# Kernel tuning notes

Hardware: AMD Instinct MI355X
Metric: run time of the kernel (lower is better)

Reference implementation:

```python
import jax, jax.numpy as jnp
import numpy as np

D_MODEL = 1024
NUM_HEADS = 16
HEAD_DIM = D_MODEL // NUM_HEADS
SCALE = HEAD_DIM ** -0.5


def setup_inputs() -> dict:
    key = jax.random.key(0)
    ks = jax.random.split(key, 5)
    B, N = 2, 2048
    x = jax.random.normal(ks[0], (B, N, D_MODEL), dtype=jnp.float32)
    # Linear params, torch layout: weight [out, in], bias [out]
    w_qkv = jax.random.normal(ks[1], (3 * D_MODEL, D_MODEL), dtype=jnp.float32) * (D_MODEL ** -0.5)
    b_qkv = jax.random.normal(ks[2], (3 * D_MODEL,), dtype=jnp.float32) * 0.02
    w_proj = jax.random.normal(ks[3], (D_MODEL, D_MODEL), dtype=jnp.float32) * (D_MODEL ** -0.5)
    b_proj = jax.random.normal(ks[4], (D_MODEL,), dtype=jnp.float32) * 0.02
    return {"x": x, "w_qkv": w_qkv, "b_qkv": b_qkv, "w_proj": w_proj, "b_proj": b_proj}


def reference(x, w_qkv, b_qkv, w_proj, b_proj):
    B, N, C = x.shape
    qkv = x @ w_qkv.T + b_qkv                      # [B, N, 3C]
    qkv = qkv.reshape(B, N, 3, NUM_HEADS, HEAD_DIM)
    qkv = jnp.transpose(qkv, (2, 0, 3, 1, 4))      # [3, B, H, N, d]
    q, k, v = qkv[0], qkv[1], qkv[2]
    attn = jnp.einsum('bhnd,bhmd->bhnm', q, k) * SCALE  # [B, H, N, N]
    attn = jax.nn.softmax(attn, axis=-1)
    # dropout is identity in eval mode
    out = jnp.einsum('bhnm,bhmd->bhnd', attn, v)   # [B, H, N, d]
    out = jnp.transpose(out, (0, 2, 1, 3)).reshape(B, N, C)
    return out @ w_proj.T + b_proj
```

## Files before the change

### kernel.cpp

```cpp
#include <hip/hip_runtime.h>

typedef short short8 __attribute__((ext_vector_type(8)));
typedef short short4v __attribute__((ext_vector_type(4)));
typedef float f32x4 __attribute__((ext_vector_type(4)));
typedef float float4v __attribute__((ext_vector_type(4)));
typedef int int4v __attribute__((ext_vector_type(4)));
typedef int int2v __attribute__((ext_vector_type(2)));

__device__ __forceinline__ short f2bf(float f) {
  union { float f; unsigned u; } v; v.f = f;
  unsigned r = v.u + 0x7FFFu + ((v.u >> 16) & 1u);
  return (short)(r >> 16);
}

__device__ __forceinline__ unsigned cvtpk_bf16(float lo, float hi) {
  unsigned r;
  asm("v_cvt_pk_bf16_f32 %0, %1, %2" : "=v"(r) : "v"(lo), "v"(hi));
  return r;
}

#define GLD16(gp, lp)                                                   \
  __builtin_amdgcn_global_load_lds(                                     \
      (const __attribute__((address_space(1))) void*)(gp),              \
      (__attribute__((address_space(3))) void*)(lp), 16, 0, 0)

#define QSCALE 0.18033688011112042f

__global__ __launch_bounds__(256) void cvt_all(
    const float* __restrict__ x, const float* __restrict__ wq, const float* __restrict__ wp,
    short* __restrict__ xb, short* __restrict__ wqb, short* __restrict__ wpb) {
  int i = blockIdx.x * 256 + threadIdx.x;
  const float* s; short* d; int off;
  if (i < 1048576)      { s = x;  d = xb;  off = i; }
  else if (i < 1835008) { s = wq; d = wqb; off = i - 1048576; }
  else                  { s = wp; d = wpb; off = i - 1835008; }
  float4v v = ((const float4v*)s)[off];
  short4v o;
  o.x = f2bf(v.x); o.y = f2bf(v.y); o.z = f2bf(v.z); o.w = f2bf(v.w);
  ((short4v*)d)[off] = o;
}

template <int MODE>
__global__ __launch_bounds__(256) void gemm_bt(
    const short* __restrict__ A, const short* __restrict__ Bw,
    const float* __restrict__ bias,
    short* __restrict__ qo, short* __restrict__ ko, short* __restrict__ vto,
    float* __restrict__ outf) {
  __shared__ short As[2][128 * 64];
  __shared__ short Bs[2][128 * 64];
  const int t = threadIdx.x;
  const int lane = t & 63, wid = t >> 6;
  const int g = lane >> 4, l15 = lane & 15;
  const int wr = (wid >> 1) * 64, wc = (wid & 1) * 64;
  const int bm0 = blockIdx.y * 128, bn0 = blockIdx.x * 128;

  const int sr = t >> 3;
  const int ssub0 = t & 7;

  const int swz = (l15 & 7) << 4;
  int aoff[2][4], boff[2][4];
#pragma unroll
  for (int kk = 0; kk < 2; ++kk)
#pragma unroll
    for (int f = 0; f < 4; ++f) {
      aoff[kk][f] = ((wr + f * 16 + l15) * 128 + kk * 64 + g * 16) ^ swz;
      boff[kk][f] = ((wc + f * 16 + l15) * 128 + kk * 64 + g * 16) ^ swz;
    }

  f32x4 acc[4][4] = {};

  auto stage = [&](int buf, int k0) {
#pragma unroll
    for (int i = 0; i < 4; ++i) {
      int row = i * 32 + sr;
      int s = ssub0 ^ (row & 7);
      char* ldsA = (char*)&As[buf][0] + (i * 256 + (t & ~63)) * 16;
      char* ldsB = (char*)&Bs[buf][0] + (i * 256 + (t & ~63)) * 16;
      GLD16(A + (size_t)(bm0 + row) * 1024 + k0 + s * 8, ldsA);
      GLD16(Bw + (size_t)(bn0 + row) * 1024 + k0 + s * 8, ldsB);
    }
  };

  stage(0, 0);
  stage(1, 64);
  int curOff = 0;

  for (int it = 0; it < 16; ++it) {
    if (it == 15) asm volatile("s_waitcnt vmcnt(0)" ::: "memory");
    else          asm volatile("s_waitcnt vmcnt(8)" ::: "memory");
    __builtin_amdgcn_s_barrier();
    __builtin_amdgcn_sched_barrier(0);
    const char* AsB = (const char*)&As[0][0] + curOff;
    const char* BsB = (const char*)&Bs[0][0] + curOff;
#pragma unroll
    for (int kk = 0; kk < 2; ++kk) {
      short8 a[4], b[4];
#pragma unroll
      for (int mi = 0; mi < 4; ++mi) a[mi] = *(const short8*)(AsB + aoff[kk][mi]);
#pragma unroll
      for (int ni = 0; ni < 4; ++ni) b[ni] = *(const short8*)(BsB + boff[kk][ni]);
#pragma unroll
      for (int mi = 0; mi < 4; ++mi)
#pragma unroll
        for (int ni = 0; ni < 4; ++ni)
          acc[mi][ni] = __builtin_amdgcn_mfma_f32_16x16x32_bf16(a[mi], b[ni], acc[mi][ni], 0, 0, 0);
    }
    __builtin_amdgcn_sched_barrier(0);
    __builtin_amdgcn_s_barrier();
    __builtin_amdgcn_sched_barrier(0);
    if (it + 2 < 16) stage(it & 1, (it + 2) * 64);
    curOff ^= 16384;
  }

  if constexpr (MODE == 0) {
    const int which = bn0 >> 10;
    if (which == 2) {
#pragma unroll
      for (int mi = 0; mi < 4; ++mi) {
#pragma unroll
        for (int ni = 0; ni < 4; ++ni) {
          int gcol = bn0 + wc + ni * 16 + l15;
          int w1 = gcol & 1023;
          int h = w1 >> 6, dd = w1 & 63;
          float bv = bias[gcol];
          int grow0 = bm0 + wr + mi * 16 + g * 4;
          int b_ = grow0 >> 11, n0 = grow0 & 2047;
          int bh = b_ * 16 + h;
          int nl = n0 & 63;
          int np = (n0 & ~63) | (nl & 32) | ((nl & 12) << 1) | ((nl & 16) >> 2);
          int2v pk;
          pk.x = (int)cvtpk_bf16(acc[mi][ni][0] + bv, acc[mi][ni][1] + bv);
          pk.y = (int)cvtpk_bf16(acc[mi][ni][2] + bv, acc[mi][ni][3] + bv);
          *(int2v*)(vto + ((size_t)bh * 64 + dd) * 2048 + np) = pk;
        }
      }
    } else {
      short* dst = (which == 0) ? qo : ko;
      const float sc = (which == 0) ? QSCALE : 1.0f;
#pragma unroll
      for (int mi = 0; mi < 4; ++mi) {
#pragma unroll
        for (int ni = 0; ni < 4; ++ni) {
          int gcol = bn0 + wc + ni * 16 + l15;
          int w1 = gcol & 1023;
          int h = w1 >> 6, dd = w1 & 63;
          float bv = bias[gcol];
#pragma unroll
          for (int r = 0; r < 4; ++r) {
            int grow = bm0 + wr + mi * 16 + g * 4 + r;
            int b_ = grow >> 11, n = grow & 2047;
            int bh = b_ * 16 + h;
            dst[((size_t)bh * 2048 + n) * 64 + dd] = f2bf((acc[mi][ni][r] + bv) * sc);
          }
        }
      }
    }
  } else {
#pragma unroll
    for (int mi = 0; mi < 4; ++mi) {
#pragma unroll
      for (int ni = 0; ni < 4; ++ni) {
        int gcol = bn0 + wc + ni * 16 + l15;
        float bv = bias[gcol];
#pragma unroll
        for (int r = 0; r < 4; ++r) {
          int grow = bm0 + wr + mi * 16 + g * 4 + r;
          outf[(size_t)grow * 1024 + gcol] = acc[mi][ni][r] + bv;
        }
      }
    }
  }
}

__global__ __launch_bounds__(256, 2) void attn_fused(
    const short* __restrict__ Qg, const short* __restrict__ Kg,
    const short* __restrict__ Vtg, short* __restrict__ AO) {
  __shared__ short Ks[4][64 * 64];
  __shared__ short Vs[4][64 * 64];
  const int bid = blockIdx.x;
  const int bh = bid & 31, qt = bid >> 5;
  const int t = threadIdx.x, wid = t >> 6, lane = t & 63;
  const int g = lane >> 4, l15 = lane & 15;
  const int q0w = qt * 128 + wid * 32;
  const short* qb = Qg + ((size_t)bh * 2048 + q0w) * 64;
  const short* kb = Kg + (size_t)bh * 2048 * 64;
  const short* vb = Vtg + (size_t)bh * 64 * 2048;

  const int srow = t >> 3;
  const int ssub = (t & 7) ^ (srow & 7);
  const short* ksrc0 = kb + srow * 64 + ssub * 8;
  const short* vsrc0 = vb + (size_t)srow * 2048 + ssub * 8;

  const int swz = (l15 & 7) << 4;
  int foff[2][4];
#pragma unroll
  for (int kk = 0; kk < 2; ++kk)
#pragma unroll
    for (int f = 0; f < 4; ++f)
      foff[kk][f] = ((f * 16 + l15) * 128 + kk * 64 + g * 16) ^ swz;

  short8 bq[2][2];
#pragma unroll
  for (int qf = 0; qf < 2; ++qf)
#pragma unroll
    for (int kk = 0; kk < 2; ++kk)
      bq[qf][kk] = *(const short8*)(qb + (qf * 16 + l15) * 64 + kk * 32 + g * 8);

  auto stageP = [&](int buf, int p) {
    const int n0 = p * 128;
#pragma unroll
    for (int sub = 0; sub < 2; ++sub) {
      const int nn = n0 + sub * 64;
      char* ldsK = (char*)&Ks[buf * 2 + sub][0] + wid * 1024;
      char* ldsV = (char*)&Vs[buf * 2 + sub][0] + wid * 1024;
#pragma unroll
      for (int i = 0; i < 2; ++i) {
        GLD16(ksrc0 + (size_t)(nn + i * 32) * 64, ldsK + i * 4096);
        GLD16(vsrc0 + (size_t)i * 32 * 2048 + nn, ldsV + i * 4096);
      }
    }
  };

  stageP(0, 0);
  stageP(1, 1);

  f32x4 acc[2][4] = {};
  float mrun[2] = {-3.0e38f, -3.0e38f}, lrun[2] = {0.f, 0.f};

  for (int p = 0; p < 16; ++p) {
    if (p == 15) asm volatile("s_waitcnt vmcnt(0)" ::: "memory");
    else         asm volatile("s_waitcnt vmcnt(8)" ::: "memory");
    __builtin_amdgcn_s_barrier();
    __builtin_amdgcn_sched_barrier(0);
    const int buf = p & 1;

#pragma unroll
    for (int sub = 0; sub < 2; ++sub) {
      const char* KsB = (const char*)&Ks[buf * 2 + sub][0];
      const char* VsB = (const char*)&Vs[buf * 2 + sub][0];

      f32x4 s[2][4] = {};
#pragma unroll
      for (int kk = 0; kk < 2; ++kk) {
        short8 ak[4];
#pragma unroll
        for (int kf = 0; kf < 4; ++kf) ak[kf] = *(const short8*)(KsB + foff[kk][kf]);
#pragma unroll
        for (int kf = 0; kf < 4; ++kf)
#pragma unroll
          for (int qf = 0; qf < 2; ++qf)
            s[qf][kf] = __builtin_amdgcn_mfma_f32_16x16x32_bf16(ak[kf], bq[qf][kk], s[qf][kf], 0, 0, 0);
      }

      float pm[2];
#pragma unroll
      for (int qf = 0; qf < 2; ++qf) {
        float m0 = fmaxf(s[qf][0][0], s[qf][0][1]);
        m0 = fmaxf(fmaxf(m0, s[qf][0][2]), s[qf][0][3]);
#pragma unroll
        for (int kf = 1; kf < 4; ++kf) {
          m0 = fmaxf(fmaxf(m0, s[qf][kf][0]), s[qf][kf][1]);
          m0 = fmaxf(fmaxf(m0, s[qf][kf][2]), s[qf][kf][3]);
        }
        float x = fmaxf(m0, __shfl_xor(m0, 16));
        pm[qf] = fmaxf(x, __shfl_xor(x, 32));
      }

      if (!__all((pm[0] - mrun[0] <= 8.f) && (pm[1] - mrun[1] <= 8.f))) {
#pragma unroll
        for (int qf = 0; qf < 2; ++qf) {
          float mn = fmaxf(mrun[qf], pm[qf]);
          float alpha = __builtin_amdgcn_exp2f(mrun[qf] - mn);
          mrun[qf] = mn;
          lrun[qf] *= alpha;
#pragma unroll
          for (int df = 0; df < 4; ++df)
#pragma unroll
            for (int r = 0; r < 4; ++r) acc[qf][df][r] *= alpha;
        }
      }

      unsigned wpk[2][4][2];
#pragma unroll
      for (int qf = 0; qf < 2; ++qf) {
        float rs = 0.f;
        float pp[4][4];
#pragma unroll
        for (int kf = 0; kf < 4; ++kf)
#pragma unroll
          for (int r = 0; r < 4; ++r) {
            pp[kf][r] = __builtin_amdgcn_exp2f(s[qf][kf][r] - mrun[qf]);
            rs += pp[kf][r];
          }
        rs += __shfl_xor(rs, 16);
        rs += __shfl_xor(rs, 32);
        lrun[qf] += rs;
#pragma unroll
        for (int kf = 0; kf < 4; ++kf)
#pragma unroll
          for (int h = 0; h < 2; ++h)
            wpk[qf][kf][h] = cvtpk_bf16(pp[kf][2 * h], pp[kf][2 * h + 1]);
      }

#pragma unroll
      for (int kk = 0; kk < 2; ++kk) {
        short8 av[4];
#pragma unroll
        for (int df = 0; df < 4; ++df) av[df] = *(const short8*)(VsB + foff[kk][df]);
#pragma unroll
        for (int qf = 0; qf < 2; ++qf) {
          union { int4v i; short8 s; } pv;
          pv.i[0] = (int)wpk[qf][2 * kk][0];
          pv.i[1] = (int)wpk[qf][2 * kk][1];
          pv.i[2] = (int)wpk[qf][2 * kk + 1][0];
          pv.i[3] = (int)wpk[qf][2 * kk + 1][1];
#pragma unroll
          for (int df = 0; df < 4; ++df)
            acc[qf][df] = __builtin_amdgcn_mfma_f32_16x16x32_bf16(av[df], pv.s, acc[qf][df], 0, 0, 0);
        }
      }
    }

    __builtin_amdgcn_sched_barrier(0);
    __builtin_amdgcn_s_barrier();
    __builtin_amdgcn_sched_barrier(0);
    if (p + 2 < 16) stageP(buf, p + 2);
  }

  const int b_ = bh >> 4, h = bh & 15;
#pragma unroll
  for (int qf = 0; qf < 2; ++qf) {
    const float inv = 1.0f / lrun[qf];
    short* outp = AO + ((size_t)b_ * 2048 + q0w + qf * 16 + l15) * 1024 + h * 64 + g * 4;
#pragma unroll
    for (int df = 0; df < 4; ++df) {
      short4v o;
#pragma unroll
      for (int r = 0; r < 4; ++r) o[r] = f2bf(acc[qf][df][r] * inv);
      *(short4v*)(outp + df * 16) = o;
    }
  }
}

extern "C" void kernel_launch(void* const* d_in, const int* in_sizes, int n_in,
                              void* d_out, int out_size, void* d_ws, size_t ws_size,
                              hipStream_t stream) {
  const float* x = (const float*)d_in[0];
  const float* w_qkv = (const float*)d_in[1];
  const float* b_qkv = (const float*)d_in[2];
  const float* w_proj = (const float*)d_in[3];
  const float* b_proj = (const float*)d_in[4];
  float* out = (float*)d_out;
  char* ws = (char*)d_ws;

  short* xb    = (short*)(ws + (size_t)0);
  short* wqkvb = (short*)(ws + ((size_t)8 << 20));
  short* wprojb= (short*)(ws + ((size_t)14 << 20));
  short* qb    = (short*)(ws + ((size_t)16 << 20));
  short* kb    = (short*)(ws + ((size_t)24 << 20));
  short* vtb   = (short*)(ws + ((size_t)32 << 20));
  short* aob   = (short*)(ws + ((size_t)40 << 20));

  cvt_all<<<8192, 256, 0, stream>>>(x, w_qkv, w_proj, xb, wqkvb, wprojb);
  gemm_bt<0><<<dim3(24, 32), 256, 0, stream>>>(xb, wqkvb, b_qkv, qb, kb, vtb, nullptr);
  attn_fused<<<512, 256, 0, stream>>>(qb, kb, vtb, aob);
  gemm_bt<1><<<dim3(8, 32), 256, 0, stream>>>(aob, wprojb, b_proj, nullptr, nullptr, nullptr, out);
}
```

Measured before the change: 122.4 us.

## Use single-wave attention blocks with register-prefetched K and double-buffered V

The attention kernel moves from 4-wave blocks sharing K/V tiles in LDS to single-wave blocks (2048 blocks of 64 threads). K fragments are loaded straight from global memory into registers one 64-key tile ahead, and only V goes through a double-buffered LDS tile staged with async global-to-LDS loads. This removes block-wide barriers and halves LDS use per block, which should allow more blocks in flight. The cost is that K/V are no longer shared across waves, so global/L2 traffic for K and V roughly quadruples.

```diff
diff --git a/kernel.cpp b/kernel.cpp
--- a/kernel.cpp
+++ b/kernel.cpp
@@ -172,23 +172,21 @@
   }
 }
 
-__global__ __launch_bounds__(256, 2) void attn_fused(
+__global__ __launch_bounds__(64, 2) void attn_fused(
     const short* __restrict__ Qg, const short* __restrict__ Kg,
     const short* __restrict__ Vtg, short* __restrict__ AO) {
-  __shared__ short Ks[4][64 * 64];
-  __shared__ short Vs[4][64 * 64];
+  __shared__ short Vs[2][64 * 64];
   const int bid = blockIdx.x;
   const int bh = bid & 31, qt = bid >> 5;
-  const int t = threadIdx.x, wid = t >> 6, lane = t & 63;
-  const int g = lane >> 4, l15 = lane & 15;
-  const int q0w = qt * 128 + wid * 32;
+  const int t = threadIdx.x;
+  const int g = t >> 4, l15 = t & 15;
+  const int q0w = qt * 32;
   const short* qb = Qg + ((size_t)bh * 2048 + q0w) * 64;
   const short* kb = Kg + (size_t)bh * 2048 * 64;
   const short* vb = Vtg + (size_t)bh * 64 * 2048;
 
   const int srow = t >> 3;
-  const int ssub = (t & 7) ^ (srow & 7);
-  const short* ksrc0 = kb + srow * 64 + ssub * 8;
+  const int ssub = (t & 7) ^ srow;
   const short* vsrc0 = vb + (size_t)srow * 2048 + ssub * 8;
 
   const int swz = (l15 & 7) << 4;
@@ -206,126 +204,131 @@
     for (int kk = 0; kk < 2; ++kk)
       bq[qf][kk] = *(const short8*)(qb + (qf * 16 + l15) * 64 + kk * 32 + g * 8);
 
-  auto stageP = [&](int buf, int p) {
-    const int n0 = p * 128;
-#pragma unroll
-    for (int sub = 0; sub < 2; ++sub) {
-      const int nn = n0 + sub * 64;
-      char* ldsK = (char*)&Ks[buf * 2 + sub][0] + wid * 1024;
-      char* ldsV = (char*)&Vs[buf * 2 + sub][0] + wid * 1024;
-#pragma unroll
-      for (int i = 0; i < 2; ++i) {
-        GLD16(ksrc0 + (size_t)(nn + i * 32) * 64, ldsK + i * 4096);
-        GLD16(vsrc0 + (size_t)i * 32 * 2048 + nn, ldsV + i * 4096);
-      }
-    }
+  auto stageV = [&](int buf, int p) {
+    const int nn = p * 64;
+    char* lds = (char*)&Vs[buf][0];
+#pragma unroll
+    for (int i = 0; i < 8; ++i)
+      GLD16(vsrc0 + (size_t)(i * 8) * 2048 + nn, lds + i * 1024);
   };
 
-  stageP(0, 0);
-  stageP(1, 1);
+  auto loadK = [&](short8 (&ak)[2][4], int p) {
+    const short* kp = kb + (size_t)(p * 64) * 64;
+#pragma unroll
+    for (int kk = 0; kk < 2; ++kk)
+#pragma unroll
+      for (int kf = 0; kf < 4; ++kf)
+        ak[kk][kf] = *(const short8*)(kp + (kf * 16 + l15) * 64 + kk * 32 + g * 8);
+  };
 
   f32x4 acc[2][4] = {};
   float mrun[2] = {-3.0e38f, -3.0e38f}, lrun[2] = {0.f, 0.f};
-
-  for (int p = 0; p < 16; ++p) {
-    if (p == 15) asm volatile("s_waitcnt vmcnt(0)" ::: "memory");
-    else         asm volatile("s_waitcnt vmcnt(8)" ::: "memory");
-    __builtin_amdgcn_s_barrier();
-    __builtin_amdgcn_sched_barrier(0);
-    const int buf = p & 1;
-
-#pragma unroll
-    for (int sub = 0; sub < 2; ++sub) {
-      const char* KsB = (const char*)&Ks[buf * 2 + sub][0];
-      const char* VsB = (const char*)&Vs[buf * 2 + sub][0];
-
-      f32x4 s[2][4] = {};
-#pragma unroll
-      for (int kk = 0; kk < 2; ++kk) {
-        short8 ak[4];
-#pragma unroll
-        for (int kf = 0; kf < 4; ++kf) ak[kf] = *(const short8*)(KsB + foff[kk][kf]);
-#pragma unroll
-        for (int kf = 0; kf < 4; ++kf)
-#pragma unroll
-          for (int qf = 0; qf < 2; ++qf)
-            s[qf][kf] = __builtin_amdgcn_mfma_f32_16x16x32_bf16(ak[kf], bq[qf][kk], s[qf][kf], 0, 0, 0);
-      }
-
-      float pm[2];
+  short8 akA[2][4], akB[2][4];
+
+  stageV(0, 0);
+  stageV(1, 1);
+  __builtin_amdgcn_sched_barrier(0);
+  loadK(akA, 0);
+  __builtin_amdgcn_sched_barrier(0);
+
+  auto body = [&](short8 (&cur)[2][4], short8 (&nxt)[2][4], int p,
+                  bool doK, bool doV, bool last) {
+    if (last) asm volatile("s_waitcnt vmcnt(0)" ::: "memory");
+    else      asm volatile("s_waitcnt vmcnt(16)" ::: "memory");
+    __builtin_amdgcn_sched_barrier(0);
+    if (doK) loadK(nxt, p + 1);
+    __builtin_amdgcn_sched_barrier(0);
+    const char* VsB = (const char*)&Vs[p & 1][0];
+
+    f32x4 s[2][4] = {};
+#pragma unroll
+    for (int kk = 0; kk < 2; ++kk)
+#pragma unroll
+      for (int kf = 0; kf < 4; ++kf)
+#pragma unroll
+        for (int qf = 0; qf < 2; ++qf)
+          s[qf][kf] = __builtin_amdgcn_mfma_f32_16x16x32_bf16(cur[kk][kf], bq[qf][kk], s[qf][kf], 0, 0, 0);
+
+    float pm[2];
+#pragma unroll
+    for (int qf = 0; qf < 2; ++qf) {
+      float m0 = fmaxf(s[qf][0][0], s[qf][0][1]);
+      m0 = fmaxf(fmaxf(m0, s[qf][0][2]), s[qf][0][3]);
+#pragma unroll
+      for (int kf = 1; kf < 4; ++kf) {
+        m0 = fmaxf(fmaxf(m0, s[qf][kf][0]), s[qf][kf][1]);
+        m0 = fmaxf(fmaxf(m0, s[qf][kf][2]), s[qf][kf][3]);
+      }
+      float x = fmaxf(m0, __shfl_xor(m0, 16));
+      pm[qf] = fmaxf(x, __shfl_xor(x, 32));
+    }
+
+    if (!__all((pm[0] - mrun[0] <= 8.f) && (pm[1] - mrun[1] <= 8.f))) {
 #pragma unroll
       for (int qf = 0; qf < 2; ++qf) {
-        float m0 = fmaxf(s[qf][0][0], s[qf][0][1]);
-        m0 = fmaxf(fmaxf(m0, s[qf][0][2]), s[qf][0][3]);
-#pragma unroll
-        for (int kf = 1; kf < 4; ++kf) {
-          m0 = fmaxf(fmaxf(m0, s[qf][kf][0]), s[qf][kf][1]);
-          m0 = fmaxf(fmaxf(m0, s[qf][kf][2]), s[qf][kf][3]);
+        float mn = fmaxf(mrun[qf], pm[qf]);
+        float alpha = __builtin_amdgcn_exp2f(mrun[qf] - mn);
+        mrun[qf] = mn;
+        lrun[qf] *= alpha;
+#pragma unroll
+        for (int df = 0; df < 4; ++df)
+#pragma unroll
+          for (int r = 0; r < 4; ++r) acc[qf][df][r] *= alpha;
+      }
+    }
+
+    unsigned wpk[2][4][2];
+#pragma unroll
+    for (int qf = 0; qf < 2; ++qf) {
+      float rs = 0.f;
+      float pp[4][4];
+#pragma unroll
+      for (int kf = 0; kf < 4; ++kf)
+#pragma unroll
+        for (int r = 0; r < 4; ++r) {
+          pp[kf][r] = __builtin_amdgcn_exp2f(s[qf][kf][r] - mrun[qf]);
+          rs += pp[kf][r];
         }
-        float x = fmaxf(m0, __shfl_xor(m0, 16));
-        pm[qf] = fmaxf(x, __shfl_xor(x, 32));
-      }
-
-      if (!__all((pm[0] - mrun[0] <= 8.f) && (pm[1] - mrun[1] <= 8.f))) {
-#pragma unroll
-        for (int qf = 0; qf < 2; ++qf) {
-          float mn = fmaxf(mrun[qf], pm[qf]);
-          float alpha = __builtin_amdgcn_exp2f(mrun[qf] - mn);
-          mrun[qf] = mn;
-          lrun[qf] *= alpha;
-#pragma unroll
-          for (int df = 0; df < 4; ++df)
-#pragma unroll
-            for (int r = 0; r < 4; ++r) acc[qf][df][r] *= alpha;
-        }
-      }
-
-      unsigned wpk[2][4][2];
+      rs += __shfl_xor(rs, 16);
+      rs += __shfl_xor(rs, 32);
+      lrun[qf] += rs;
+#pragma unroll
+      for (int kf = 0; kf < 4; ++kf)
+#pragma unroll
+        for (int h = 0; h < 2; ++h)
+          wpk[qf][kf][h] = cvtpk_bf16(pp[kf][2 * h], pp[kf][2 * h + 1]);
+    }
+
+#pragma unroll
+    for (int kk = 0; kk < 2; ++kk) {
+      short8 av[4];
+#pragma unroll
+      for (int df = 0; df < 4; ++df) av[df] = *(const short8*)(VsB + foff[kk][df]);
 #pragma unroll
       for (int qf = 0; qf < 2; ++qf) {
-        float rs = 0.f;
-        float pp[4][4];
-#pragma unroll
-        for (int kf = 0; kf < 4; ++kf)
-#pragma unroll
-          for (int r = 0; r < 4; ++r) {
-            pp[kf][r] = __builtin_amdgcn_exp2f(s[qf][kf][r] - mrun[qf]);
-            rs += pp[kf][r];
-          }
-        rs += __shfl_xor(rs, 16);
-        rs += __shfl_xor(rs, 32);
-        lrun[qf] += rs;
-#pragma unroll
-        for (int kf = 0; kf < 4; ++kf)
-#pragma unroll
-          for (int h = 0; h < 2; ++h)
-            wpk[qf][kf][h] = cvtpk_bf16(pp[kf][2 * h], pp[kf][2 * h + 1]);
-      }
-
-#pragma unroll
-      for (int kk = 0; kk < 2; ++kk) {
-        short8 av[4];
-#pragma unroll
-        for (int df = 0; df < 4; ++df) av[df] = *(const short8*)(VsB + foff[kk][df]);
-#pragma unroll
-        for (int qf = 0; qf < 2; ++qf) {
-          union { int4v i; short8 s; } pv;
-          pv.i[0] = (int)wpk[qf][2 * kk][0];
-          pv.i[1] = (int)wpk[qf][2 * kk][1];
-          pv.i[2] = (int)wpk[qf][2 * kk + 1][0];
-          pv.i[3] = (int)wpk[qf][2 * kk + 1][1];
-#pragma unroll
-          for (int df = 0; df < 4; ++df)
-            acc[qf][df] = __builtin_amdgcn_mfma_f32_16x16x32_bf16(av[df], pv.s, acc[qf][df], 0, 0, 0);
-        }
-      }
-    }
-
-    __builtin_amdgcn_sched_barrier(0);
-    __builtin_amdgcn_s_barrier();
-    __builtin_amdgcn_sched_barrier(0);
-    if (p + 2 < 16) stageP(buf, p + 2);
+        union { int4v i; short8 s; } pv;
+        pv.i[0] = (int)wpk[qf][2 * kk][0];
+        pv.i[1] = (int)wpk[qf][2 * kk][1];
+        pv.i[2] = (int)wpk[qf][2 * kk + 1][0];
+        pv.i[3] = (int)wpk[qf][2 * kk + 1][1];
+#pragma unroll
+        for (int df = 0; df < 4; ++df)
+          acc[qf][df] = __builtin_amdgcn_mfma_f32_16x16x32_bf16(av[df], pv.s, acc[qf][df], 0, 0, 0);
+      }
+    }
+
+    asm volatile("s_waitcnt lgkmcnt(0)" ::: "memory");
+    __builtin_amdgcn_sched_barrier(0);
+    if (doV) stageV(p & 1, p + 2);
+    __builtin_amdgcn_sched_barrier(0);
+  };
+
+  for (int it2 = 0; it2 < 15; ++it2) {
+    body(akA, akB, 2 * it2,     true, true, false);
+    body(akB, akA, 2 * it2 + 1, true, true, false);
   }
+  body(akA, akB, 30, true,  false, false);
+  body(akB, akA, 31, false, false, true);
 
   const int b_ = bh >> 4, h = bh & 15;
 #pragma unroll
@@ -363,6 +366,6 @@
 
   cvt_all<<<8192, 256, 0, stream>>>(x, w_qkv, w_proj, xb, wqkvb, wprojb);
   gemm_bt<0><<<dim3(24, 32), 256, 0, stream>>>(xb, wqkvb, b_qkv, qb, kb, vtb, nullptr);
-  attn_fused<<<512, 256, 0, stream>>>(qb, kb, vtb, aob);
+  attn_fused<<<2048, 64, 0, stream>>>(qb, kb, vtb, aob);
   gemm_bt<1><<<dim3(8, 32), 256, 0, stream>>>(aob, wprojb, b_proj, nullptr, nullptr, nullptr, out);
 }
```

After: 155.5 us. 27.0% more time.

## Use triple-buffered K=32 LDS pipeline with swizzled block order in GEMMs

Applied to the files above, without the earlier changes.

Restructures both GEMM kernels from a double-buffered K=64 stage to a triple-buffered K=32 stage, cutting LDS use from 64KB to 48KB per block and raising launch bounds so three blocks can be resident. Block indices are remapped on a 1D grid so consecutive blocks share B columns and group A rows for better L2 reuse. The LDS XOR swizzle and wait counts are redone for the narrower tile. The cost is twice as many barriers per K loop and smaller MFMA batches between syncs.

```diff
diff --git a/kernel.cpp b/kernel.cpp
--- a/kernel.cpp
+++ b/kernel.cpp
@@ -41,75 +41,73 @@
 }
 
 template <int MODE>
-__global__ __launch_bounds__(256) void gemm_bt(
+__global__ __launch_bounds__(256, 3) void gemm_bt(
     const short* __restrict__ A, const short* __restrict__ Bw,
     const float* __restrict__ bias,
     short* __restrict__ qo, short* __restrict__ ko, short* __restrict__ vto,
     float* __restrict__ outf) {
-  __shared__ short As[2][128 * 64];
-  __shared__ short Bs[2][128 * 64];
+  __shared__ short As[3][128 * 32];
+  __shared__ short Bs[3][128 * 32];
   const int t = threadIdx.x;
   const int lane = t & 63, wid = t >> 6;
   const int g = lane >> 4, l15 = lane & 15;
   const int wr = (wid >> 1) * 64, wc = (wid & 1) * 64;
-  const int bm0 = blockIdx.y * 128, bn0 = blockIdx.x * 128;
-
-  const int sr = t >> 3;
-  const int ssub0 = t & 7;
-
-  const int swz = (l15 & 7) << 4;
-  int aoff[2][4], boff[2][4];
-#pragma unroll
-  for (int kk = 0; kk < 2; ++kk)
-#pragma unroll
-    for (int f = 0; f < 4; ++f) {
-      aoff[kk][f] = ((wr + f * 16 + l15) * 128 + kk * 64 + g * 16) ^ swz;
-      boff[kk][f] = ((wc + f * 16 + l15) * 128 + kk * 64 + g * 16) ^ swz;
-    }
+  const int bid = blockIdx.x;
+  const int bm0 = ((bid & 7) * 4 + ((bid >> 3) & 3)) * 128;
+  const int bn0 = (bid >> 5) * 128;
+
+  const int sr = t >> 2;
+  const int csrc = (t & 3) ^ ((t >> 3) & 3);
+
+  const int gx = (g ^ ((l15 >> 1) & 3)) << 4;
+  int aoff[4], boff[4];
+#pragma unroll
+  for (int f = 0; f < 4; ++f) {
+    aoff[f] = (wr + f * 16 + l15) * 64 + gx;
+    boff[f] = (wc + f * 16 + l15) * 64 + gx;
+  }
 
   f32x4 acc[4][4] = {};
 
-  auto stage = [&](int buf, int k0) {
-#pragma unroll
-    for (int i = 0; i < 4; ++i) {
-      int row = i * 32 + sr;
-      int s = ssub0 ^ (row & 7);
-      char* ldsA = (char*)&As[buf][0] + (i * 256 + (t & ~63)) * 16;
-      char* ldsB = (char*)&Bs[buf][0] + (i * 256 + (t & ~63)) * 16;
-      GLD16(A + (size_t)(bm0 + row) * 1024 + k0 + s * 8, ldsA);
-      GLD16(Bw + (size_t)(bn0 + row) * 1024 + k0 + s * 8, ldsB);
+  auto stage = [&](int offB, int k0) {
+#pragma unroll
+    for (int i = 0; i < 2; ++i) {
+      int row = i * 64 + sr;
+      char* ldsA = (char*)&As[0][0] + offB + (i * 256 + (t & ~63)) * 16;
+      char* ldsB = (char*)&Bs[0][0] + offB + (i * 256 + (t & ~63)) * 16;
+      GLD16(A + (size_t)(bm0 + row) * 1024 + k0 + csrc * 8, ldsA);
+      GLD16(Bw + (size_t)(bn0 + row) * 1024 + k0 + csrc * 8, ldsB);
     }
   };
 
   stage(0, 0);
-  stage(1, 64);
-  int curOff = 0;
-
-  for (int it = 0; it < 16; ++it) {
-    if (it == 15) asm volatile("s_waitcnt vmcnt(0)" ::: "memory");
-    else          asm volatile("s_waitcnt vmcnt(8)" ::: "memory");
+  stage(8192, 32);
+  stage(16384, 64);
+  int off = 0;
+
+  for (int it = 0; it < 32; ++it) {
+    if (it < 30)       asm volatile("s_waitcnt vmcnt(8)" ::: "memory");
+    else if (it == 30) asm volatile("s_waitcnt vmcnt(4)" ::: "memory");
+    else               asm volatile("s_waitcnt vmcnt(0)" ::: "memory");
     __builtin_amdgcn_s_barrier();
     __builtin_amdgcn_sched_barrier(0);
-    const char* AsB = (const char*)&As[0][0] + curOff;
-    const char* BsB = (const char*)&Bs[0][0] + curOff;
-#pragma unroll
-    for (int kk = 0; kk < 2; ++kk) {
-      short8 a[4], b[4];
-#pragma unroll
-      for (int mi = 0; mi < 4; ++mi) a[mi] = *(const short8*)(AsB + aoff[kk][mi]);
-#pragma unroll
-      for (int ni = 0; ni < 4; ++ni) b[ni] = *(const short8*)(BsB + boff[kk][ni]);
-#pragma unroll
-      for (int mi = 0; mi < 4; ++mi)
-#pragma unroll
-        for (int ni = 0; ni < 4; ++ni)
-          acc[mi][ni] = __builtin_amdgcn_mfma_f32_16x16x32_bf16(a[mi], b[ni], acc[mi][ni], 0, 0, 0);
-    }
+    const char* AsB = (const char*)&As[0][0] + off;
+    const char* BsB = (const char*)&Bs[0][0] + off;
+    short8 a[4], b[4];
+#pragma unroll
+    for (int mi = 0; mi < 4; ++mi) a[mi] = *(const short8*)(AsB + aoff[mi]);
+#pragma unroll
+    for (int ni = 0; ni < 4; ++ni) b[ni] = *(const short8*)(BsB + boff[ni]);
+#pragma unroll
+    for (int mi = 0; mi < 4; ++mi)
+#pragma unroll
+      for (int ni = 0; ni < 4; ++ni)
+        acc[mi][ni] = __builtin_amdgcn_mfma_f32_16x16x32_bf16(a[mi], b[ni], acc[mi][ni], 0, 0, 0);
     __builtin_amdgcn_sched_barrier(0);
     __builtin_amdgcn_s_barrier();
     __builtin_amdgcn_sched_barrier(0);
-    if (it + 2 < 16) stage(it & 1, (it + 2) * 64);
-    curOff ^= 16384;
+    if (it + 3 < 32) stage(off, (it + 3) * 32);
+    off = (off == 16384) ? 0 : off + 8192;
   }
 
   if constexpr (MODE == 0) {
@@ -362,7 +360,7 @@
   short* aob   = (short*)(ws + ((size_t)40 << 20));
 
   cvt_all<<<8192, 256, 0, stream>>>(x, w_qkv, w_proj, xb, wqkvb, wprojb);
-  gemm_bt<0><<<dim3(24, 32), 256, 0, stream>>>(xb, wqkvb, b_qkv, qb, kb, vtb, nullptr);
+  gemm_bt<0><<<768, 256, 0, stream>>>(xb, wqkvb, b_qkv, qb, kb, vtb, nullptr);
   attn_fused<<<512, 256, 0, stream>>>(qb, kb, vtb, aob);
-  gemm_bt<1><<<dim3(8, 32), 256, 0, stream>>>(aob, wprojb, b_proj, nullptr, nullptr, nullptr, out);
-}
+  gemm_bt<1><<<256, 256, 0, stream>>>(aob, wprojb, b_proj, nullptr, nullptr, nullptr, out);
+}
```

Result: faster. 115.7 us (-5.5%).
